# Optimization experiments

Hardware: AMD Instinct MI355X
Metric: run time of the kernel (lower is better)

## Reference

```python
import jax, jax.numpy as jnp
import numpy as np

HID, H, HKV, D, INT, S, T = 2048, 16, 8, 128, 6144, 4096, 512
POS = 0          # absolute position of the first token in this prefill chunk
EPS = 1e-6
SCALE = 1.0 / D ** 0.5
REP = H // HKV


def setup_inputs() -> dict:
    key = jax.random.key(0)
    ks = jax.random.split(key, 12)
    w = lambda k, sh: jax.random.normal(k, sh, dtype=jnp.float32) * 0.02

    hidden_conv = jax.random.normal(ks[0], (1, HID, 1, T), dtype=jnp.float32)

    # RoPE tables for absolute positions POS..POS+T-1, HF half-rotation layout
    inv_freq = 1.0 / (10000.0 ** (jnp.arange(0, D, 2, dtype=jnp.float32) / D))
    pos = (POS + jnp.arange(T, dtype=jnp.float32))
    ang = pos[:, None] * inv_freq[None, :]                      # (T, D/2)
    emb = jnp.concatenate([ang, ang], axis=-1)                  # (T, D)
    cos = jnp.cos(emb)[None]                                    # (1, T, D)
    sin = jnp.sin(emb)[None]

    # one-hot write mask: column t has a 1 at row POS+t
    update_mask = jnp.zeros((S, T), jnp.float32).at[POS + jnp.arange(T), jnp.arange(T)].set(1.0)[None, None]
    # causal mask over the cache: slot s visible to token t iff s <= POS+t
    attn_mask = jnp.where(jnp.arange(S)[None, :] <= (POS + jnp.arange(T))[:, None], 0.0, -1e4).astype(jnp.float32)[None, None]

    k_cache = jnp.zeros((1, HKV, S, D), jnp.float32)
    v_cache = jnp.zeros((1, HKV, S, D), jnp.float32)

    return dict(
        hidden_conv=hidden_conv, cos=cos, sin=sin,
        update_mask=update_mask, attn_mask=attn_mask,
        k_cache=k_cache, v_cache=v_cache,
        wq=w(ks[1], (H * D, HID)), wk=w(ks[2], (HKV * D, HID)),
        wv=w(ks[3], (HKV * D, HID)), wo=w(ks[4], (HID, H * D)),
        ln1_w=jnp.ones((HID,), jnp.float32), ln2_w=jnp.ones((HID,), jnp.float32),
        qn_w=jnp.ones((D,), jnp.float32), kn_w=jnp.ones((D,), jnp.float32),
        w_gate_up=w(ks[5], (2 * INT, HID)), w_down=w(ks[6], (HID, INT)),
    )


def _rms(x, w):
    return x * jax.lax.rsqrt(jnp.mean(x * x, axis=-1, keepdims=True) + EPS) * w


def _rotate_half(x):
    x1, x2 = jnp.split(x, 2, axis=-1)
    return jnp.concatenate([-x2, x1], axis=-1)


def reference(hidden_conv, cos, sin, update_mask, attn_mask, k_cache, v_cache,
              wq, wk, wv, wo, ln1_w, ln2_w, qn_w, kn_w, w_gate_up, w_down):
    # (1, HID, 1, T) conv layout -> (1, T, HID)
    x = jnp.transpose(hidden_conv[:, :, 0, :], (0, 2, 1))

    h = _rms(x, ln1_w)
    # 1x1 conv == linear; channel order h*D+d matches view(1,H,D,T)
    q = jnp.einsum('btc,oc->bto', h, wq).reshape(1, T, H, D).transpose(0, 2, 1, 3)    # (1,H,T,D)
    k = jnp.einsum('btc,oc->bto', h, wk).reshape(1, T, HKV, D).transpose(0, 2, 1, 3)  # (1,HKV,T,D)
    v = jnp.einsum('btc,oc->bto', h, wv).reshape(1, T, HKV, D).transpose(0, 2, 1, 3)

    q = _rms(q, qn_w)
    k = _rms(k, kn_w)

    cos_b = cos[:, None]  # (1,1,T,D)
    sin_b = sin[:, None]
    q = q * cos_b + _rotate_half(q) * sin_b
    k = k * cos_b + _rotate_half(k) * sin_b

    # matmul-based KV cache write via one-hot mask (faithful to original)
    k_inc = jnp.matmul(update_mask, k)                 # (1,HKV,S,D)
    v_inc = jnp.matmul(update_mask, v)
    write_any = jnp.sum(update_mask, axis=-1, keepdims=True)  # (1,1,S,1)
    k_full = k_cache * (1.0 - write_any) + k_inc
    v_full = v_cache * (1.0 - write_any) + v_inc

    k_rep = jnp.repeat(k_full, REP, axis=1)            # (1,H,S,D)
    v_rep = jnp.repeat(v_full, REP, axis=1)

    scores = jnp.einsum('bhtd,bhsd->bhts', q, k_rep) * SCALE + attn_mask  # (1,H,T,S)
    attn = jax.nn.softmax(scores, axis=-1)
    out = jnp.einsum('bhts,bhsd->bhtd', attn, v_rep)   # (1,H,T,D)

    o_in = out.transpose(0, 2, 1, 3).reshape(1, T, H * D)
    attn_out = jnp.einsum('btc,oc->bto', o_in, wo)
    hidden = x + attn_out

    h2 = _rms(hidden, ln2_w)
    gate_up = jnp.einsum('btc,oc->bto', h2, w_gate_up)
    gate, up = jnp.split(gate_up, 2, axis=-1)
    mlp = jnp.einsum('bti,oi->bto', jax.nn.silu(gate) * up, w_down)
    hidden = hidden + mlp

    hidden_out = jnp.transpose(hidden, (0, 2, 1))[:, :, None, :]  # back to (1,HID,1,T)
    return hidden_out, k_full, v_full


if __name__ == '__main__':
    outs = reference(**setup_inputs())
    print([o.shape for o in outs])
```

## Files before the change

### kernel.cpp

```cpp
#include <hip/hip_runtime.h>
#include <hip/hip_bf16.h>

#define TT 512
#define HIDD 2048
#define NH 16
#define NKV 8
#define DD 128
#define INTR 6144
#define SEQ 4096
#define SCALE 0.08838834764831845f

typedef __attribute__((ext_vector_type(8))) short short8;
typedef __attribute__((ext_vector_type(4))) float floatx4;

static __device__ __forceinline__ unsigned short f2b(float f) {
  unsigned int u = __float_as_uint(f);
  u += 0x7fffu + ((u >> 16) & 1u);
  return (unsigned short)(u >> 16);
}

static __device__ __forceinline__ unsigned int f2b2(float a, float b) {
  __hip_bfloat162 h = __float22bfloat162_rn(make_float2(a, b));
  return *reinterpret_cast<unsigned int*>(&h);
}


template <int BM, bool H> struct TR;
template <> struct TR<128, true>  { short8 v[2]; };
template <> struct TR<128, false> { float4 v[4]; };
template <> struct TR<64, true>   { short8 v[1]; };
template <> struct TR<64, false>  { float4 v[2]; };

template <int BM, bool H>
static __device__ __forceinline__ void tile_load(const void* __restrict__ src, int ld, int k0,
                                                 int tid, TR<BM, H>& r) {
  if constexpr (H) {
    const unsigned short* s = (const unsigned short*)src;
    const int r0 = tid >> 2, c8 = (tid & 3) << 3;
#pragma unroll
    for (int i = 0; i < BM / 64; ++i)
      r.v[i] = *reinterpret_cast<const short8*>(s + (size_t)(r0 + (i << 6)) * ld + k0 + c8);
  } else {
    const float* s = (const float*)src;
    const int r0 = tid >> 3, c4 = (tid & 7) << 2;
#pragma unroll
    for (int i = 0; i < BM / 32; ++i)
      r.v[i] = *reinterpret_cast<const float4*>(s + (size_t)(r0 + (i << 5)) * ld + k0 + c4);
  }
}

template <int BM, bool H>
static __device__ __forceinline__ void tile_store(const TR<BM, H>& r, unsigned short* dst, int tid) {
  if constexpr (H) {
    const int r0 = tid >> 2, c8 = (tid & 3) << 3;
#pragma unroll
    for (int i = 0; i < BM / 64; ++i)
      *reinterpret_cast<short8*>(dst + (r0 + (i << 6)) * 40 + c8) = r.v[i];
  } else {
    const int r0 = tid >> 3, c4 = (tid & 7) << 2;
#pragma unroll
    for (int i = 0; i < BM / 32; ++i) {
      uint2 o;
      o.x = f2b2(r.v[i].x, r.v[i].y);
      o.y = f2b2(r.v[i].z, r.v[i].w);
      *reinterpret_cast<uint2*>(dst + (r0 + (i << 5)) * 40 + c4) = o;
    }
  }
}

template <int BM, bool A16, bool B16>
static __device__ __forceinline__ void gemm_core(const void* __restrict__ A, int lda,
                                                 const void* __restrict__ B, int ldb,
                                                 int kbeg, int kend, floatx4 (&acc)[BM / 32][4],
                                                 unsigned short* As, unsigned short* Bs) {
  constexpr int MI = BM / 32;
  const int tid = threadIdx.x;
  const int lane = tid & 63;
  const int wave = tid >> 6;
  const int wr = (wave >> 1) * (BM >> 1);
  const int wc = (wave & 1) << 6;
  const int lrow = lane & 15;
  const int koff = (lane >> 4) << 3;
  TR<BM, A16> ra;
  TR<128, B16> rb;
  tile_load<BM, A16>(A, lda, kbeg, tid, ra);
  tile_load<128, B16>(B, ldb, kbeg, tid, rb);
  tile_store<BM, A16>(ra, As, tid);
  tile_store<128, B16>(rb, Bs, tid);
  if (kbeg + 32 < kend) {
    tile_load<BM, A16>(A, lda, kbeg + 32, tid, ra);
    tile_load<128, B16>(B, ldb, kbeg + 32, tid, rb);
  }
  __syncthreads();
  int p = 0;
  for (int k0 = kbeg; k0 < kend; k0 += 32) {
    const unsigned short* Ac = As + p * (BM * 40);
    const unsigned short* Bc = Bs + p * (128 * 40);
    unsigned short* An = As + (p ^ 1) * (BM * 40);
    unsigned short* Bn = Bs + (p ^ 1) * (128 * 40);
    short8 af[MI], bfr[4];
#pragma unroll
    for (int mi = 0; mi < MI; ++mi)
      af[mi] = *reinterpret_cast<const short8*>(Ac + (wr + mi * 16 + lrow) * 40 + koff);
#pragma unroll
    for (int ni = 0; ni < 4; ++ni)
      bfr[ni] = *reinterpret_cast<const short8*>(Bc + (wc + ni * 16 + lrow) * 40 + koff);
    if (k0 + 32 < kend) {
      tile_store<BM, A16>(ra, An, tid);
      tile_store<128, B16>(rb, Bn, tid);
      if (k0 + 64 < kend) {
        tile_load<BM, A16>(A, lda, k0 + 64, tid, ra);
        tile_load<128, B16>(B, ldb, k0 + 64, tid, rb);
      }
    }
#pragma unroll
    for (int mi = 0; mi < MI; ++mi)
#pragma unroll
      for (int ni = 0; ni < 4; ++ni)
        acc[mi][ni] = __builtin_amdgcn_mfma_f32_16x16x32_bf16(af[mi], bfr[ni], acc[mi][ni], 0, 0, 0);
    __syncthreads();
    p ^= 1;
  }
}

#define EPI_VARS \
  const int lane = threadIdx.x & 63; \
  const int wave = threadIdx.x >> 6; \
  const int wc = (wave & 1) << 6;    \
  const int lrow = lane & 15;        \
  const int quad = lane >> 4;

#define ZERO_ACC(MI_) \
  floatx4 acc[MI_][4]; \
  _Pragma("unroll") for (int mi = 0; mi < MI_; ++mi) \
  _Pragma("unroll") for (int ni = 0; ni < 4; ++ni) { floatx4 z = {0.f, 0.f, 0.f, 0.f}; acc[mi][ni] = z; }

template <int S>
static __device__ __forceinline__ void swz(int b, int& mt, int& nt, int& s) {
  mt = (b >> 3) & 3;
  const int gid = ((b >> 5) << 3) | (b & 7);
  nt = gid / S;
  s = gid - nt * S;
}


__global__ __launch_bounds__(1024) void k_rms1(const float* __restrict__ conv,
                                               const float* __restrict__ w,
                                               float* __restrict__ xb,
                                               unsigned short* __restrict__ h1b) {
  const int t0 = blockIdx.x << 5;
  const int tid = threadIdx.x;
  const int j = tid & 31;
  const int g = tid >> 5;
  __shared__ float part[32][32];
  __shared__ float tile[32][33];
  __shared__ float rs[32];
  float ss = 0.f;
  for (int c0 = 0; c0 < HIDD; c0 += 32) {
    const float v = conv[(size_t)(c0 + g) * TT + t0 + j];
    ss += v * v;
  }
  part[g][j] = ss;
  __syncthreads();
  if (g == 0) {
    float tot = 0.f;
#pragma unroll
    for (int q = 0; q < 32; ++q) tot += part[q][j];
    rs[j] = rsqrtf(tot * (1.0f / HIDD) + 1e-6f);
  }
  __syncthreads();
  for (int c0 = 0; c0 < HIDD; c0 += 32) {
    tile[g][j] = conv[(size_t)(c0 + g) * TT + t0 + j];
    __syncthreads();
    const float v = tile[j][g];
    const float rv = rs[g];
    xb[(size_t)(t0 + g) * HIDD + c0 + j] = v;
    h1b[(size_t)(t0 + g) * HIDD + c0 + j] = f2b(v * rv * w[c0 + j]);
    __syncthreads();
  }
}

__global__ __launch_bounds__(256) void k_gemm_qkv(const unsigned short* __restrict__ h1b,
                                                  const float* __restrict__ wq,
                                                  const float* __restrict__ wk,
                                                  const float* __restrict__ wv,
                                                  float* __restrict__ Pq) {
  __shared__ unsigned short As[2 * 128 * 40], Bs[2 * 128 * 40];
  int mt, nt, s;
  swz<4>(blockIdx.x, mt, nt, s);
  const int m0 = mt << 7, n0 = nt << 7;
  const float* Bp;
  if (n0 < 2048)      Bp = wq + (size_t)n0 * HIDD;
  else if (n0 < 3072) Bp = wk + (size_t)(n0 - 2048) * HIDD;
  else                Bp = wv + (size_t)(n0 - 3072) * HIDD;
  ZERO_ACC(4)
  gemm_core<128, true, false>(h1b + (size_t)m0 * HIDD, HIDD, Bp, HIDD, s * 512, s * 512 + 512, acc, As, Bs);
  EPI_VARS
  const int wr = (wave >> 1) << 6;
  float* out = Pq + (size_t)s * (TT * 4096);
#pragma unroll
  for (int mi = 0; mi < 4; ++mi)
#pragma unroll
    for (int ni = 0; ni < 4; ++ni)
#pragma unroll
      for (int rr = 0; rr < 4; ++rr) {
        const int row = m0 + wr + mi * 16 + quad * 4 + rr;
        const int col = n0 + wc + ni * 16 + lrow;
        out[(size_t)row * 4096 + col] = acc[mi][ni][rr];
      }
}

__global__ __launch_bounds__(128) void k_rope(const float* __restrict__ Pq,
                                              const float* __restrict__ cosb,
                                              const float* __restrict__ sinb,
                                              const float* __restrict__ qnw,
                                              const float* __restrict__ knw,
                                              unsigned short* __restrict__ qb,
                                              unsigned short* __restrict__ kb,
                                              unsigned short* __restrict__ vtb,
                                              float* __restrict__ kout,
                                              float* __restrict__ vout) {
  const int u = blockIdx.x;
  const int t = blockIdx.y;
  const int d = threadIdx.x;
  __shared__ float red[2];
  __shared__ float sh[DD];
  int slot;
  if (u < NH)            slot = u * DD + d;
  else if (u < NH + NKV) slot = 2048 + (u - NH) * DD + d;
  else                   slot = 3072 + (u - NH - NKV) * DD + d;
  const size_t idx = (size_t)t * 4096 + slot;
  float val = Pq[idx] + Pq[idx + TT * 4096] + Pq[idx + 2 * TT * 4096] + Pq[idx + 3 * TT * 4096];
  if (u < NH + NKV) {
    float ss = val * val;
    const int lane = d & 63, wid = d >> 6;
#pragma unroll
    for (int o = 32; o; o >>= 1) ss += __shfl_xor(ss, o);
    if (!lane) red[wid] = ss;
    __syncthreads();
    const float r = rsqrtf((red[0] + red[1]) * (1.0f / DD) + 1e-6f);
    const float w = (u < NH) ? qnw[d] : knw[d];
    const float nv = val * r * w;
    sh[d] = nv;
    __syncthreads();
    const float partner = sh[d ^ 64];
    const float rh = (d < 64) ? -partner : partner;
    const float o = nv * cosb[(size_t)t * DD + d] + rh * sinb[(size_t)t * DD + d];
    if (u < NH) {
      qb[(size_t)u * TT * DD + (size_t)t * DD + d] = f2b(o);
    } else {
      const int kh = u - NH;
      kout[(size_t)kh * SEQ * DD + (size_t)t * DD + d] = o;
      kb[(size_t)kh * TT * DD + (size_t)t * DD + d] = f2b(o);
    }
  } else {
    const int vh = u - NH - NKV;
    vout[(size_t)vh * SEQ * DD + (size_t)t * DD + d] = val;
    vtb[(size_t)vh * DD * TT + (size_t)d * TT + t] = f2b(val);
  }
}

__global__ __launch_bounds__(256) void k_tail(const float* __restrict__ kc,
                                              const float* __restrict__ vc,
                                              float* __restrict__ ko,
                                              float* __restrict__ vo) {
  const int i = blockIdx.x * 256 + threadIdx.x;
  const int e = i << 2;
  const int s = (e >> 7) & (SEQ - 1);
  if (s >= TT) {
    reinterpret_cast<float4*>(ko)[i] = reinterpret_cast<const float4*>(kc)[i];
    reinterpret_cast<float4*>(vo)[i] = reinterpret_cast<const float4*>(vc)[i];
  }
}

__global__ __launch_bounds__(256) void k_scores(const unsigned short* __restrict__ qb,
                                                const unsigned short* __restrict__ kb,
                                                float* __restrict__ sc) {
  __shared__ unsigned short As[2 * 64 * 40], Bs[2 * 128 * 40];
  const int m0 = blockIdx.x << 6, n0 = blockIdx.y << 7, h = blockIdx.z;
  ZERO_ACC(2)
  gemm_core<64, true, true>(qb + (size_t)h * TT * DD + (size_t)m0 * DD, DD,
                            kb + (size_t)(h >> 1) * TT * DD + (size_t)n0 * DD, DD, 0, DD, acc, As, Bs);
  EPI_VARS
  const int wr = (wave >> 1) << 5;
  float* out = sc + (size_t)h * TT * TT;
#pragma unroll
  for (int mi = 0; mi < 2; ++mi)
#pragma unroll
    for (int ni = 0; ni < 4; ++ni)
#pragma unroll
      for (int rr = 0; rr < 4; ++rr) {
        const int t = m0 + wr + mi * 16 + quad * 4 + rr;
        const int s = n0 + wc + ni * 16 + lrow;
        float v = acc[mi][ni][rr] * SCALE;
        if (s > t) v += -10000.0f;
        out[(size_t)t * TT + s] = v;
      }
}

__global__ __launch_bounds__(256) void k_softmax(const float* __restrict__ sc,
                                                 unsigned short* __restrict__ Pb) {
  const int h = blockIdx.x >> 9, t = blockIdx.x & 511;
  const int tid = threadIdx.x;
  const float* row = sc + ((size_t)h * TT + t) * TT;
  float v0 = row[tid], v1 = row[tid + 256];
  __shared__ float red[4];
  const int lane = tid & 63, wid = tid >> 6;
  float m = fmaxf(v0, v1);
#pragma unroll
  for (int o = 32; o; o >>= 1) m = fmaxf(m, __shfl_xor(m, o));
  if (!lane) red[wid] = m;
  __syncthreads();
  m = fmaxf(fmaxf(red[0], red[1]), fmaxf(red[2], red[3]));
  const float e0 = __expf(v0 - m), e1 = __expf(v1 - m);
  float s = e0 + e1;
  __syncthreads();
#pragma unroll
  for (int o = 32; o; o >>= 1) s += __shfl_xor(s, o);
  if (!lane) red[wid] = s;
  __syncthreads();
  const float inv = 1.0f / (red[0] + red[1] + red[2] + red[3]);
  unsigned short* orow = Pb + ((size_t)h * TT + t) * TT;
  orow[tid] = f2b(e0 * inv);
  orow[tid + 256] = f2b(e1 * inv);
}

__global__ __launch_bounds__(256) void k_pv(const unsigned short* __restrict__ Pb,
                                            const unsigned short* __restrict__ vtb,
                                            float* __restrict__ Ppv) {
  __shared__ unsigned short As[2 * 64 * 40], Bs[2 * 128 * 40];
  const int m0 = blockIdx.x << 6, h = blockIdx.y, s = blockIdx.z;
  ZERO_ACC(2)
  gemm_core<64, true, true>(Pb + (size_t)h * TT * TT + (size_t)m0 * TT, TT,
                            vtb + (size_t)(h >> 1) * DD * TT, TT, s * 128, s * 128 + 128, acc, As, Bs);
  EPI_VARS
  const int wr = (wave >> 1) << 5;
  float* out = Ppv + (size_t)s * (TT * HIDD);
#pragma unroll
  for (int mi = 0; mi < 2; ++mi)
#pragma unroll
    for (int ni = 0; ni < 4; ++ni)
#pragma unroll
      for (int rr = 0; rr < 4; ++rr) {
        const int row = m0 + wr + mi * 16 + quad * 4 + rr;
        const int col = wc + ni * 16 + lrow;
        out[(size_t)row * HIDD + h * DD + col] = acc[mi][ni][rr];
      }
}

__global__ __launch_bounds__(256) void k_red_pv(const float* __restrict__ Ppv,
                                                unsigned short* __restrict__ o_inb) {
  const int i = blockIdx.x * 256 + threadIdx.x;
  const float4* p = reinterpret_cast<const float4*>(Ppv);
  float4 a = p[i];
  const float4 b = p[i + 262144], c = p[i + 524288], d = p[i + 786432];
  a.x += b.x + c.x + d.x; a.y += b.y + c.y + d.y;
  a.z += b.z + c.z + d.z; a.w += b.w + c.w + d.w;
  uint2 o;
  o.x = f2b2(a.x, a.y);
  o.y = f2b2(a.z, a.w);
  *reinterpret_cast<uint2*>(o_inb + (size_t)i * 4) = o;
}

__global__ __launch_bounds__(256) void k_gemm_o(const unsigned short* __restrict__ o_inb,
                                                const float* __restrict__ wo,
                                                float* __restrict__ Po) {
  __shared__ unsigned short As[2 * 128 * 40], Bs[2 * 128 * 40];
  int mt, nt, s;
  swz<8>(blockIdx.x, mt, nt, s);
  const int m0 = mt << 7, n0 = nt << 7;
  ZERO_ACC(4)
  gemm_core<128, true, false>(o_inb + (size_t)m0 * HIDD, HIDD, wo + (size_t)n0 * HIDD, HIDD,
                              s * 256, s * 256 + 256, acc, As, Bs);
  EPI_VARS
  const int wr = (wave >> 1) << 6;
  float* out = Po + (size_t)s * (TT * HIDD);
#pragma unroll
  for (int mi = 0; mi < 4; ++mi)
#pragma unroll
    for (int ni = 0; ni < 4; ++ni)
#pragma unroll
      for (int rr = 0; rr < 4; ++rr) {
        const int row = m0 + wr + mi * 16 + quad * 4 + rr;
        const int col = n0 + wc + ni * 16 + lrow;
        out[(size_t)row * HIDD + col] = acc[mi][ni][rr];
      }
}

__global__ __launch_bounds__(256) void k_rms2(const float* __restrict__ xb,
                                              const float* __restrict__ Po,
                                              const float* __restrict__ w,
                                              float* __restrict__ hidden,
                                              unsigned short* __restrict__ h2b) {
  const int t = blockIdx.x;
  const int tid = threadIdx.x;
  float2 v[4];
  float ss = 0.f;
#pragma unroll
  for (int i = 0; i < 4; ++i) {
    const int c = (tid << 1) + (i << 9);
    const size_t idx = (size_t)t * HIDD + c;
    float2 a = *reinterpret_cast<const float2*>(xb + idx);
#pragma unroll
    for (int sp = 0; sp < 8; ++sp) {
      const float2 b = *reinterpret_cast<const float2*>(Po + idx + (size_t)sp * (TT * HIDD));
      a.x += b.x; a.y += b.y;
    }
    v[i] = a;
    ss += a.x * a.x + a.y * a.y;
  }
  __shared__ float red[4];
  const int lane = tid & 63, wid = tid >> 6;
#pragma unroll
  for (int o = 32; o; o >>= 1) ss += __shfl_xor(ss, o);
  if (!lane) red[wid] = ss;
  __syncthreads();
  const float tot = red[0] + red[1] + red[2] + red[3];
  const float r = rsqrtf(tot * (1.0f / HIDD) + 1e-6f);
#pragma unroll
  for (int i = 0; i < 4; ++i) {
    const int c = (tid << 1) + (i << 9);
    const size_t idx = (size_t)t * HIDD + c;
    *reinterpret_cast<float2*>(hidden + idx) = v[i];
    const float2 wv2 = *reinterpret_cast<const float2*>(w + c);
    *reinterpret_cast<unsigned int*>(h2b + idx) = f2b2(v[i].x * r * wv2.x, v[i].y * r * wv2.y);
  }
}

__global__ __launch_bounds__(256) void k_gemm_gu(const unsigned short* __restrict__ h2b,
                                                 const float* __restrict__ wgu,
                                                 float* __restrict__ gu) {
  __shared__ unsigned short As[2 * 64 * 40], Bs[2 * 128 * 40];
  const int bid = blockIdx.x;
  const int mt = bid / 96, nt = bid - mt * 96;
  const int m0 = mt << 6, n0 = nt << 7;
  ZERO_ACC(2)
  gemm_core<64, true, false>(h2b + (size_t)m0 * HIDD, HIDD, wgu + (size_t)n0 * HIDD, HIDD,
                             0, HIDD, acc, As, Bs);
  EPI_VARS
  const int wr = (wave >> 1) << 5;
#pragma unroll
  for (int mi = 0; mi < 2; ++mi)
#pragma unroll
    for (int ni = 0; ni < 4; ++ni)
#pragma unroll
      for (int rr = 0; rr < 4; ++rr) {
        const int row = m0 + wr + mi * 16 + quad * 4 + rr;
        const int col = n0 + wc + ni * 16 + lrow;
        gu[(size_t)row * (2 * INTR) + col] = acc[mi][ni][rr];
      }
}

__global__ __launch_bounds__(256) void k_silu(const float* __restrict__ gu,
                                              unsigned short* __restrict__ actb) {
  const int j0 = (blockIdx.x * 256 + threadIdx.x) << 1;
  const int t = blockIdx.y;
  const float2 g = *reinterpret_cast<const float2*>(gu + (size_t)t * (2 * INTR) + j0);
  const float2 u = *reinterpret_cast<const float2*>(gu + (size_t)t * (2 * INTR) + INTR + j0);
  const float a0 = g.x / (1.f + __expf(-g.x)) * u.x;
  const float a1 = g.y / (1.f + __expf(-g.y)) * u.y;
  *reinterpret_cast<unsigned int*>(actb + (size_t)t * INTR + j0) = f2b2(a0, a1);
}

__global__ __launch_bounds__(256) void k_gemm_down(const unsigned short* __restrict__ actb,
                                                   const float* __restrict__ wdn,
                                                   float* __restrict__ Pdn) {
  __shared__ unsigned short As[2 * 128 * 40], Bs[2 * 128 * 40];
  int mt, nt, s;
  swz<8>(blockIdx.x, mt, nt, s);
  const int m0 = mt << 7, n0 = nt << 7;
  ZERO_ACC(4)
  gemm_core<128, true, false>(actb + (size_t)m0 * INTR, INTR, wdn + (size_t)n0 * INTR, INTR,
                              s * 768, s * 768 + 768, acc, As, Bs);
  EPI_VARS
  const int wr = (wave >> 1) << 6;
  float* out = Pdn + (size_t)s * (TT * HIDD);
#pragma unroll
  for (int mi = 0; mi < 4; ++mi)
#pragma unroll
    for (int ni = 0; ni < 4; ++ni)
#pragma unroll
      for (int rr = 0; rr < 4; ++rr) {
        const int row = m0 + wr + mi * 16 + quad * 4 + rr;
        const int col = n0 + wc + ni * 16 + lrow;
        out[(size_t)row * HIDD + col] = acc[mi][ni][rr];
      }
}

__global__ __launch_bounds__(256) void k_final(const float* __restrict__ hidden,
                                               const float* __restrict__ Pdn,
                                               float* __restrict__ out0) {
  __shared__ float tile[32][33];
  const int c0 = blockIdx.x << 5, t0 = blockIdx.y << 5;
  const int tx = threadIdx.x & 31, ty0 = (threadIdx.x >> 5) << 2;
#pragma unroll
  for (int i = 0; i < 4; ++i) {
    const int t = t0 + ty0 + i;
    const size_t idx = (size_t)t * HIDD + c0 + tx;
    float a = hidden[idx];
#pragma unroll
    for (int sp = 0; sp < 8; ++sp) a += Pdn[idx + (size_t)sp * (TT * HIDD)];
    tile[ty0 + i][tx] = a;
  }
  __syncthreads();
#pragma unroll
  for (int i = 0; i < 4; ++i)
    out0[(size_t)(c0 + ty0 + i) * TT + t0 + tx] = tile[tx][ty0 + i];
}

extern "C" void kernel_launch(void* const* d_in, const int* in_sizes, int n_in,
                              void* d_out, int out_size, void* d_ws, size_t ws_size,
                              hipStream_t stream) {
  const float* conv   = (const float*)d_in[0];
  const float* cosb   = (const float*)d_in[1];
  const float* sinb   = (const float*)d_in[2];
  const float* kcache = (const float*)d_in[5];
  const float* vcache = (const float*)d_in[6];
  const float* wq  = (const float*)d_in[7];
  const float* wk  = (const float*)d_in[8];
  const float* wv  = (const float*)d_in[9];
  const float* wo  = (const float*)d_in[10];
  const float* ln1 = (const float*)d_in[11];
  const float* ln2 = (const float*)d_in[12];
  const float* qnw = (const float*)d_in[13];
  const float* knw = (const float*)d_in[14];
  const float* wgu = (const float*)d_in[15];
  const float* wdn = (const float*)d_in[16];

  float* ws = (float*)d_ws;
  float* xb = ws + 0;
  unsigned short* h1b  = (unsigned short*)(ws + 1048576);
  unsigned short* o_inb = h1b;
  unsigned short* h2b  = (unsigned short*)(ws + 1572864);
  float* hidden = ws + 2097152;
  unsigned short* qb  = (unsigned short*)(ws + 3145728);
  unsigned short* kb  = qb + 1048576;
  unsigned short* vtb = kb + 524288;
  unsigned short* actb = (unsigned short*)(ws + 4194304);
  float* R   = ws + 5767168;
  float* Pq  = R;
  unsigned short* Pb = (unsigned short*)R;
  float* sc  = R + 2097152;
  float* Ppv = R + 2097152;
  float* Po  = R;
  float* gu  = R;
  float* Pdn = R;

  float* out0 = (float*)d_out;
  float* kout = out0 + 1048576;
  float* vout = kout + 4194304;

  k_rms1<<<16, 1024, 0, stream>>>(conv, ln1, xb, h1b);
  k_gemm_qkv<<<512, 256, 0, stream>>>(h1b, wq, wk, wv, Pq);
  k_rope<<<dim3(NH + 2 * NKV, TT), 128, 0, stream>>>(Pq, cosb, sinb, qnw, knw, qb, kb, vtb, kout, vout);
  k_tail<<<4096, 256, 0, stream>>>(kcache, vcache, kout, vout);
  k_scores<<<dim3(8, 4, NH), 256, 0, stream>>>(qb, kb, sc);
  k_softmax<<<NH * TT, 256, 0, stream>>>(sc, Pb);
  k_pv<<<dim3(8, NH, 4), 256, 0, stream>>>(Pb, vtb, Ppv);
  k_red_pv<<<1024, 256, 0, stream>>>(Ppv, o_inb);
  k_gemm_o<<<512, 256, 0, stream>>>(o_inb, wo, Po);
  k_rms2<<<TT, 256, 0, stream>>>(xb, Po, ln2, hidden, h2b);
  k_gemm_gu<<<768, 256, 0, stream>>>(h2b, wgu, gu);
  k_silu<<<dim3(12, TT), 256, 0, stream>>>(gu, actb);
  k_gemm_down<<<512, 256, 0, stream>>>(actb, wdn, Pdn);
  k_final<<<dim3(HIDD / 32, TT / 32), 256, 0, stream>>>(hidden, Pdn, out0);
}
```

Baseline: 484.4 us.

## Split-K gate/up GEMM with 128x128 tiles, fp16 partials, and wider fp32 tile loads

The gate/up GEMM moves from 64x128 tiles over the full K to 128x128 tiles with a two-way split-K. Each split writes fp16 partial sums, and the SiLU kernel now adds the two partials before the activation. The fp32 tile load/store path is also reorganized so each thread loads 8 consecutive floats and writes one 16-byte LDS store instead of two 8-byte ones; this affects every GEMM that reads fp32 weights. The aim is better per-tile data reuse, less partial-buffer traffic, and fewer shared-memory store instructions, at the cost of fp16 rounding of the partials (with a possible overflow risk) and an extra read in the SiLU kernel.

```diff
diff --git a/kernel.cpp b/kernel.cpp
--- a/kernel.cpp
+++ b/kernel.cpp
@@ -1,5 +1,6 @@
 #include <hip/hip_runtime.h>
 #include <hip/hip_bf16.h>
+#include <hip/hip_fp16.h>
 
 #define TT 512
 #define HIDD 2048
@@ -42,10 +43,13 @@
       r.v[i] = *reinterpret_cast<const short8*>(s + (size_t)(r0 + (i << 6)) * ld + k0 + c8);
   } else {
     const float* s = (const float*)src;
-    const int r0 = tid >> 3, c4 = (tid & 7) << 2;
-#pragma unroll
-    for (int i = 0; i < BM / 32; ++i)
-      r.v[i] = *reinterpret_cast<const float4*>(s + (size_t)(r0 + (i << 5)) * ld + k0 + c4);
+    const int r0 = tid >> 2, c8 = (tid & 3) << 3;
+#pragma unroll
+    for (int i = 0; i < BM / 64; ++i) {
+      const float* p = s + (size_t)(r0 + (i << 6)) * ld + k0 + c8;
+      r.v[2 * i]     = *reinterpret_cast<const float4*>(p);
+      r.v[2 * i + 1] = *reinterpret_cast<const float4*>(p + 4);
+    }
   }
 }
 
@@ -57,13 +61,15 @@
     for (int i = 0; i < BM / 64; ++i)
       *reinterpret_cast<short8*>(dst + (r0 + (i << 6)) * 40 + c8) = r.v[i];
   } else {
-    const int r0 = tid >> 3, c4 = (tid & 7) << 2;
-#pragma unroll
-    for (int i = 0; i < BM / 32; ++i) {
-      uint2 o;
-      o.x = f2b2(r.v[i].x, r.v[i].y);
-      o.y = f2b2(r.v[i].z, r.v[i].w);
-      *reinterpret_cast<uint2*>(dst + (r0 + (i << 5)) * 40 + c4) = o;
+    const int r0 = tid >> 2, c8 = (tid & 3) << 3;
+#pragma unroll
+    for (int i = 0; i < BM / 64; ++i) {
+      uint4 o;
+      o.x = f2b2(r.v[2 * i].x,     r.v[2 * i].y);
+      o.y = f2b2(r.v[2 * i].z,     r.v[2 * i].w);
+      o.z = f2b2(r.v[2 * i + 1].x, r.v[2 * i + 1].y);
+      o.w = f2b2(r.v[2 * i + 1].z, r.v[2 * i + 1].w);
+      *reinterpret_cast<uint4*>(dst + (r0 + (i << 6)) * 40 + c8) = o;
     }
   }
 }
@@ -429,36 +435,43 @@
 
 __global__ __launch_bounds__(256) void k_gemm_gu(const unsigned short* __restrict__ h2b,
                                                  const float* __restrict__ wgu,
-                                                 float* __restrict__ gu) {
-  __shared__ unsigned short As[2 * 64 * 40], Bs[2 * 128 * 40];
-  const int bid = blockIdx.x;
-  const int mt = bid / 96, nt = bid - mt * 96;
-  const int m0 = mt << 6, n0 = nt << 7;
-  ZERO_ACC(2)
-  gemm_core<64, true, false>(h2b + (size_t)m0 * HIDD, HIDD, wgu + (size_t)n0 * HIDD, HIDD,
-                             0, HIDD, acc, As, Bs);
+                                                 __half* __restrict__ guh) {
+  __shared__ unsigned short As[2 * 128 * 40], Bs[2 * 128 * 40];
+  int mt, nt, s;
+  swz<2>(blockIdx.x, mt, nt, s);
+  const int m0 = mt << 7, n0 = nt << 7;
+  ZERO_ACC(4)
+  gemm_core<128, true, false>(h2b + (size_t)m0 * HIDD, HIDD, wgu + (size_t)n0 * HIDD, HIDD,
+                              s * 1024, s * 1024 + 1024, acc, As, Bs);
   EPI_VARS
-  const int wr = (wave >> 1) << 5;
-#pragma unroll
-  for (int mi = 0; mi < 2; ++mi)
+  const int wr = (wave >> 1) << 6;
+  __half* out = guh + (size_t)s * (TT * 2 * INTR);
+#pragma unroll
+  for (int mi = 0; mi < 4; ++mi)
 #pragma unroll
     for (int ni = 0; ni < 4; ++ni)
 #pragma unroll
       for (int rr = 0; rr < 4; ++rr) {
         const int row = m0 + wr + mi * 16 + quad * 4 + rr;
         const int col = n0 + wc + ni * 16 + lrow;
-        gu[(size_t)row * (2 * INTR) + col] = acc[mi][ni][rr];
-      }
-}
-
-__global__ __launch_bounds__(256) void k_silu(const float* __restrict__ gu,
+        out[(size_t)row * (2 * INTR) + col] = __float2half(acc[mi][ni][rr]);
+      }
+}
+
+__global__ __launch_bounds__(256) void k_silu(const __half* __restrict__ guh,
                                               unsigned short* __restrict__ actb) {
   const int j0 = (blockIdx.x * 256 + threadIdx.x) << 1;
   const int t = blockIdx.y;
-  const float2 g = *reinterpret_cast<const float2*>(gu + (size_t)t * (2 * INTR) + j0);
-  const float2 u = *reinterpret_cast<const float2*>(gu + (size_t)t * (2 * INTR) + INTR + j0);
-  const float a0 = g.x / (1.f + __expf(-g.x)) * u.x;
-  const float a1 = g.y / (1.f + __expf(-g.y)) * u.y;
+  const size_t base = (size_t)t * (2 * INTR) + j0;
+  const size_t off = (size_t)TT * (2 * INTR);
+  const float2 g0 = __half22float2(*reinterpret_cast<const __half2*>(guh + base));
+  const float2 g1 = __half22float2(*reinterpret_cast<const __half2*>(guh + off + base));
+  const float2 u0 = __half22float2(*reinterpret_cast<const __half2*>(guh + base + INTR));
+  const float2 u1 = __half22float2(*reinterpret_cast<const __half2*>(guh + off + base + INTR));
+  const float gx = g0.x + g1.x, gy = g0.y + g1.y;
+  const float ux = u0.x + u1.x, uy = u0.y + u1.y;
+  const float a0 = gx / (1.f + __expf(-gx)) * ux;
+  const float a1 = gy / (1.f + __expf(-gy)) * uy;
   *reinterpret_cast<unsigned int*>(actb + (size_t)t * INTR + j0) = f2b2(a0, a1);
 }
 
@@ -543,7 +556,7 @@
   float* sc  = R + 2097152;
   float* Ppv = R + 2097152;
   float* Po  = R;
-  float* gu  = R;
+  __half* guh = (__half*)R;
   float* Pdn = R;
 
   float* out0 = (float*)d_out;
@@ -560,8 +573,8 @@
   k_red_pv<<<1024, 256, 0, stream>>>(Ppv, o_inb);
   k_gemm_o<<<512, 256, 0, stream>>>(o_inb, wo, Po);
   k_rms2<<<TT, 256, 0, stream>>>(xb, Po, ln2, hidden, h2b);
-  k_gemm_gu<<<768, 256, 0, stream>>>(h2b, wgu, gu);
-  k_silu<<<dim3(12, TT), 256, 0, stream>>>(gu, actb);
+  k_gemm_gu<<<768, 256, 0, stream>>>(h2b, wgu, guh);
+  k_silu<<<dim3(12, TT), 256, 0, stream>>>(guh, actb);
   k_gemm_down<<<512, 256, 0, stream>>>(actb, wdn, Pdn);
   k_final<<<dim3(HIDD / 32, TT / 32), 256, 0, stream>>>(hidden, Pdn, out0);
 }
```

Result: no change. 479.6 us (-1.0%).
